# Optimization experiments

Hardware: AMD Instinct MI355X
Metric: run time of the kernel (lower is better)

The kernel has to match this reference:

```python
import jax, jax.numpy as jnp
import numpy as np

B, C_IN, L = 64, 8, 8192
ENC, K, CD = 64, 128, 64  # encoder_dim, codebook_size, code_dim


def setup_inputs() -> dict:
    key = jax.random.key(0)
    ks = jax.random.split(key, 12)
    u = lambda k, s, lim: jax.random.uniform(k, s, jnp.float32, -lim, lim)
    return {
        "x": jax.random.normal(ks[0], (B, C_IN, L), jnp.float32),
        "conv1_w": u(ks[1], (32, C_IN, 5), 1.0 / np.sqrt(C_IN * 5)),
        "conv1_b": u(ks[2], (32,), 1.0 / np.sqrt(C_IN * 5)),
        "conv2_w": u(ks[3], (ENC, 32, 5), 1.0 / np.sqrt(32 * 5)),
        "conv2_b": u(ks[4], (ENC,), 1.0 / np.sqrt(32 * 5)),
        "codebook": jax.random.uniform(ks[5], (K, CD), jnp.float32, -0.1, 0.1),
        "gru_w_ih": u(ks[6], (3 * ENC, CD), 1.0 / np.sqrt(ENC)),
        "gru_w_hh": u(ks[7], (3 * ENC, ENC), 1.0 / np.sqrt(ENC)),
        "gru_b_ih": u(ks[8], (3 * ENC,), 1.0 / np.sqrt(ENC)),
        "gru_b_hh": u(ks[9], (3 * ENC,), 1.0 / np.sqrt(ENC)),
        "proj_w": u(ks[10], (CD, ENC), 1.0 / np.sqrt(ENC)),
        "proj_b": u(ks[11], (CD,), 1.0 / np.sqrt(ENC)),
    }


def _conv1d(x, w, b):
    # x: [B, Cin, L], w: [Cout, Cin, 5], stride 2, padding 2
    y = jax.lax.conv_general_dilated(
        x, w, window_strides=(2,), padding=[(2, 2)],
        dimension_numbers=("NCH", "OIH", "NCH"))
    return y + b[None, :, None]


def _quantize(z, codebook):
    # z: [B, T, D]; squared-distance argmin + straight-through
    Bz, T, D = z.shape
    flat = z.reshape(Bz * T, D)
    flat_sg = jax.lax.stop_gradient(flat)
    cb_sg = jax.lax.stop_gradient(codebook)
    dist = ((flat_sg ** 2).sum(-1, keepdims=True)
            + (cb_sg ** 2).sum(-1)[None, :]
            - 2.0 * flat_sg @ cb_sg.T)  # [B*T, K]
    codes = jnp.argmin(dist, axis=1).reshape(Bz, T)
    quant = codebook[codes]  # [B, T, D]
    quant_z = z + jax.lax.stop_gradient(quant - z)
    return quant_z, codes


def _gru(seq, w_ih, w_hh, b_ih, b_hh):
    # seq: [B, T, CD] -> outputs [B, T, ENC]; torch GRU gate math
    Bz, T, _ = seq.shape
    H = w_hh.shape[1]
    x_proj = seq @ w_ih.T + b_ih  # [B, T, 3H]
    x_proj = jnp.transpose(x_proj, (1, 0, 2))  # [T, B, 3H]

    def step(h, xt):
        gh = h @ w_hh.T + b_hh
        xr, xz, xn = jnp.split(xt, 3, axis=-1)
        hr, hz, hn = jnp.split(gh, 3, axis=-1)
        r = jax.nn.sigmoid(xr + hr)
        zg = jax.nn.sigmoid(xz + hz)
        n = jnp.tanh(xn + r * hn)
        h_new = (1.0 - zg) * n + zg * h
        return h_new, h_new

    h0 = jnp.zeros((Bz, H), seq.dtype)
    _, hs = jax.lax.scan(step, h0, x_proj)
    return jnp.transpose(hs, (1, 0, 2))  # [B, T, H]


def reference(x, conv1_w, conv1_b, conv2_w, conv2_b, codebook,
              gru_w_ih, gru_w_hh, gru_b_ih, gru_b_hh, proj_w, proj_b):
    z = jax.nn.relu(_conv1d(x, conv1_w, conv1_b))
    z = jax.nn.relu(_conv1d(z, conv2_w, conv2_b))
    z = jnp.transpose(z, (0, 2, 1))  # [B, T, ENC]
    quant_z, codes = _quantize(z, codebook)
    ctx = _gru(quant_z, gru_w_ih, gru_w_hh, gru_b_ih, gru_b_hh)
    pred = ctx @ proj_w.T + proj_b
    return quant_z, pred, codes
```

## Files before the change

kernel.cpp:

```cpp
#include <hip/hip_runtime.h>

#define NB   64
#define CIN  8
#define LIN  8192
#define L1N  4096
#define T2   2048
#define ENC  64
#define NK   128
#define CD   64
#define G3   192

#define QOFF 0
#define POFF 8388608
#define COFF 16777216

#define PCOFF 128
#define CIOFF 24704

typedef _Float16 half2v __attribute__((ext_vector_type(2)));

__device__ __forceinline__ float sigf(float x) {
  float e = __builtin_amdgcn_exp2f(-1.4426950408889634f * x);
  return __builtin_amdgcn_rcpf(1.0f + e);
}
__device__ __forceinline__ float tanhf_fast(float x) {
  float e = __builtin_amdgcn_exp2f(2.8853900817779268f * x);
  return 1.0f - 2.0f * __builtin_amdgcn_rcpf(e + 1.0f);
}
__device__ __forceinline__ float rlane(float v, int k) {
  return __int_as_float(__builtin_amdgcn_readlane(__float_as_int(v), k));
}
__device__ __forceinline__ half2v as_h2(float v) { return __builtin_bit_cast(half2v, v); }

__global__ __launch_bounds__(192) void prep_kernel(const float* __restrict__ cb,
                                                   const float* __restrict__ w_ih,
                                                   const float* __restrict__ b_ih,
                                                   float* __restrict__ cnorm,
                                                   float* __restrict__ PC) {
  int blk = blockIdx.x;
  int j = threadIdx.x;
  if (blk == 128) {
    if (j < 128) {
      const float4* r = (const float4*)(cb + j * CD);
      float s0 = 0.f, s1 = 0.f, s2 = 0.f, s3 = 0.f;
#pragma unroll
      for (int q = 0; q < 16; q += 4) {
        float4 a = r[q], b = r[q + 1], cc = r[q + 2], d = r[q + 3];
        s0 += a.x * a.x + a.y * a.y + a.z * a.z + a.w * a.w;
        s1 += b.x * b.x + b.y * b.y + b.z * b.z + b.w * b.w;
        s2 += cc.x * cc.x + cc.y * cc.y + cc.z * cc.z + cc.w * cc.w;
        s3 += d.x * d.x + d.y * d.y + d.z * d.z + d.w * d.w;
      }
      cnorm[j] = (s0 + s1) + (s2 + s3);
    }
    return;
  }
  int c = blk;
  const float4* wp = (const float4*)(w_ih + j * ENC);
  const float4* cp = (const float4*)(cb + c * CD);
  float a0 = b_ih[j], a1 = 0.f, a2 = 0.f, a3 = 0.f;
#pragma unroll
  for (int q = 0; q < 16; q += 4) {
    float4 w0 = wp[q], c0 = cp[q];
    float4 w1 = wp[q + 1], c1 = cp[q + 1];
    float4 w2 = wp[q + 2], c2 = cp[q + 2];
    float4 w3 = wp[q + 3], c3 = cp[q + 3];
    a0 += w0.x * c0.x + w0.y * c0.y + w0.z * c0.z + w0.w * c0.w;
    a1 += w1.x * c1.x + w1.y * c1.y + w1.z * c1.z + w1.w * c1.w;
    a2 += w2.x * c2.x + w2.y * c2.y + w2.z * c2.z + w2.w * c2.w;
    a3 += w3.x * c3.x + w3.y * c3.y + w3.z * c3.z + w3.w * c3.w;
  }
  PC[c * G3 + j] = (a0 + a1) + (a2 + a3);
}

__global__ __launch_bounds__(256) void conv1_kernel(const float* __restrict__ x,
                                                    const float* __restrict__ w1,
                                                    const float* __restrict__ b1,
                                                    float* __restrict__ y1) {
  __shared__ float sw[1280];
  __shared__ float sx[8][136];
  int b = blockIdx.x >> 6;
  int t0 = (blockIdx.x & 63) * 64;
  int tid = threadIdx.x;
  for (int i = tid; i < 1280; i += 256) sw[i] = w1[i];
  const float* xb = x + b * CIN * LIN;
  for (int i = tid; i < 8 * 131; i += 256) {
    int ci = i / 131, u = i - ci * 131;
    int xi = 2 * t0 - 2 + u;
    sx[ci][u] = ((unsigned)xi < (unsigned)LIN) ? xb[ci * LIN + xi] : 0.f;
  }
  __syncthreads();
  int co = tid >> 3, tg = tid & 7;
  float bias = b1[co];
  float acc[8];
#pragma unroll
  for (int j = 0; j < 8; j++) acc[j] = bias;
#pragma unroll
  for (int ci = 0; ci < 8; ci++) {
    float xv[20];
    const float2* s2 = (const float2*)(&sx[ci][16 * tg]);
#pragma unroll
    for (int q = 0; q < 10; q++) {
      float2 v = s2[q];
      xv[2 * q] = v.x; xv[2 * q + 1] = v.y;
    }
    float wk[5];
#pragma unroll
    for (int k = 0; k < 5; k++) wk[k] = sw[(co * 8 + ci) * 5 + k];
#pragma unroll
    for (int j = 0; j < 8; j++) {
#pragma unroll
      for (int k = 0; k < 5; k++) acc[j] = fmaf(xv[2 * j + k], wk[k], acc[j]);
    }
  }
  float4* outp = (float4*)(y1 + (b * 32 + co) * L1N + t0 + tg * 8);
  float4 o0, o1;
  o0.x = fmaxf(acc[0], 0.f); o0.y = fmaxf(acc[1], 0.f);
  o0.z = fmaxf(acc[2], 0.f); o0.w = fmaxf(acc[3], 0.f);
  o1.x = fmaxf(acc[4], 0.f); o1.y = fmaxf(acc[5], 0.f);
  o1.z = fmaxf(acc[6], 0.f); o1.w = fmaxf(acc[7], 0.f);
  outp[0] = o0; outp[1] = o1;
}

__global__ __launch_bounds__(256) void conv2q_kernel(const float* __restrict__ y1,
                                                     const float* __restrict__ w2,
                                                     const float* __restrict__ b2,
                                                     const float* __restrict__ cb,
                                                     const float* __restrict__ cnorm,
                                                     float* __restrict__ quant,
                                                     float* __restrict__ codes_f,
                                                     int* __restrict__ codes_i) {
  __shared__ float sw[32 * 5 * 64];
  __shared__ float sx[32][136];
  __shared__ float sz[64][64];
  int b = blockIdx.x >> 5;
  int t0 = (blockIdx.x & 31) * 64;
  int tid = threadIdx.x;
  for (int i = tid; i < 32 * 5 * 64; i += 256) {
    int co = i & 63, r = i >> 6;
    sw[i] = w2[co * 160 + r];
  }
  for (int i = tid; i < 32 * 136; i += 256) {
    int ci = i / 136, u = i - ci * 136;
    int xi = 2 * t0 - 4 + u;
    float v = 0.f;
    if (xi >= 0 && xi < L1N) v = y1[(b * 32 + ci) * L1N + xi];
    sx[ci][u] = v;
  }
  __syncthreads();
  int co = tid & 63, ts = tid >> 6;
  float acc[16];
  float bb = b2[co];
#pragma unroll
  for (int i = 0; i < 16; i++) acc[i] = bb;
  for (int ci = 0; ci < 32; ci++) {
    float xr[40];
    const float4* sx4 = (const float4*)(&sx[ci][32 * ts]);
#pragma unroll
    for (int q = 0; q < 10; q++) {
      float4 v = sx4[q];
      xr[4 * q] = v.x; xr[4 * q + 1] = v.y; xr[4 * q + 2] = v.z; xr[4 * q + 3] = v.w;
    }
    float wk[5];
#pragma unroll
    for (int k = 0; k < 5; k++) wk[k] = sw[(ci * 5 + k) * 64 + co];
#pragma unroll
    for (int i = 0; i < 16; i++) {
#pragma unroll
      for (int k = 0; k < 5; k++) acc[i] = fmaf(xr[2 * i + k + 2], wk[k], acc[i]);
    }
  }
#pragma unroll
  for (int i = 0; i < 16; i++) sz[ts * 16 + i][co] = fmaxf(acc[i], 0.f);
  __syncthreads();

  int lane = co, wave = ts;
  float4 ca[16], cq[16];
  {
    const float4* pa = (const float4*)(cb + lane * CD);
    const float4* pb = (const float4*)(cb + (64 + lane) * CD);
#pragma unroll
    for (int q = 0; q < 16; q++) { ca[q] = pa[q]; cq[q] = pb[q]; }
  }
  float cn0 = cnorm[lane], cn1 = cnorm[64 + lane];
  int vg0 = b * T2 + t0 + wave * 16;
  for (int i = 0; i < 16; i++) {
    int vl = wave * 16 + i;
    int v = vg0 + i;
    float d00 = 0.f, d01 = 0.f, d02 = 0.f, d03 = 0.f;
    float d10 = 0.f, d11 = 0.f, d12 = 0.f, d13 = 0.f;
#pragma unroll
    for (int q = 0; q < 16; q++) {
      float4 zq = *(const float4*)(&sz[vl][4 * q]);
      d00 = fmaf(ca[q].x, zq.x, d00); d01 = fmaf(ca[q].y, zq.y, d01);
      d02 = fmaf(ca[q].z, zq.z, d02); d03 = fmaf(ca[q].w, zq.w, d03);
      d10 = fmaf(cq[q].x, zq.x, d10); d11 = fmaf(cq[q].y, zq.y, d11);
      d12 = fmaf(cq[q].z, zq.z, d12); d13 = fmaf(cq[q].w, zq.w, d13);
    }
    float s0 = cn0 - 2.f * ((d00 + d01) + (d02 + d03));
    float s1 = cn1 - 2.f * ((d10 + d11) + (d12 + d13));
    float sc; int idx;
    if (s1 < s0) { sc = s1; idx = 64 + lane; } else { sc = s0; idx = lane; }
#pragma unroll
    for (int m = 1; m < 64; m <<= 1) {
      float os = __shfl_xor(sc, m);
      int oi = __shfl_xor(idx, m);
      if (os < sc || (os == sc && oi < idx)) { sc = os; idx = oi; }
    }
    if (lane == 0) { codes_f[v] = (float)idx; codes_i[v] = idx; }
    quant[v * 64 + lane] = cb[idx * 64 + lane];
  }
}

__global__ __attribute__((amdgpu_flat_work_group_size(256, 256), amdgpu_waves_per_eu(1, 1)))
void gruproj_kernel(const float* __restrict__ PC,
                    const int* __restrict__ codes_i,
                    const float* __restrict__ w_hh,
                    const float* __restrict__ b_hh,
                    const float* __restrict__ proj_w,
                    const float* __restrict__ proj_b,
                    float* __restrict__ pred) {
  __shared__ float pcl[NK * G3];
  __shared__ int   cpl[T2];
  __shared__ float hring[2][16][64];
  int b = blockIdx.x;
  int tid = threadIdx.x;
  int lane = tid & 63;
  int wq = tid >> 6;

  {
    const int4* src = (const int4*)(codes_i + b * T2);
    int4* dst = (int4*)cpl;
    for (int f = tid; f < T2 / 4; f += 256) dst[f] = src[f];
    const float4* s2 = (const float4*)PC;
    float4* d2 = (float4*)pcl;
    for (int f = tid; f < NK * G3 / 4; f += 256) d2[f] = s2[f];
  }
  __syncthreads();

  half2v wr[32], wz[32], wn[32];
  float br = 0.f, bz = 0.f, bn = 0.f;
  float hreg = 0.f;
  int c2 = 0;
  float xr0 = 0.f, xz0 = 0.f, xn0 = 0.f, xr1 = 0.f, xz1 = 0.f, xn1 = 0.f;
  float4 w[16];
  float pbias = 0.f;

  if (wq == 0) {
    const float2* p0 = (const float2*)(w_hh + lane * ENC);
    const float2* p1 = (const float2*)(w_hh + (64 + lane) * ENC);
    const float2* p2 = (const float2*)(w_hh + (128 + lane) * ENC);
#pragma unroll
    for (int m = 0; m < 32; m++) {
      float2 a = p0[m]; wr[m] = (half2v){(_Float16)a.x, (_Float16)a.y};
      float2 c = p1[m]; wz[m] = (half2v){(_Float16)c.x, (_Float16)c.y};
      float2 d = p2[m]; wn[m] = (half2v){(_Float16)d.x, (_Float16)d.y};
    }
    br = b_hh[lane]; bz = b_hh[64 + lane]; bn = b_hh[128 + lane];
    c2 = cpl[2];
    int c0 = cpl[0], c1 = cpl[1];
    const float* g = pcl + c0 * G3;
    xr0 = g[lane]; xz0 = g[64 + lane]; xn0 = g[128 + lane];
    g = pcl + c1 * G3;
    xr1 = g[lane]; xz1 = g[64 + lane]; xn1 = g[128 + lane];
  } else {
    const float4* wp = (const float4*)(proj_w + lane * ENC);
#pragma unroll
    for (int q = 0; q < 16; q++) w[q] = wp[q];
    pbias = proj_b[lane];
  }

  int lane2a = 2 * lane, lane2b = 2 * lane + 1;
  const int cmax = T2 - 1;
  float* pbase = pred + (size_t)b * T2 * ENC + lane;

#pragma unroll 1
  for (int c = 0; c < 128; c++) {
    if (wq == 0) {
#pragma unroll 1
      for (int i = 0; i < 16; i++) {
        int t = c * 16 + i;
        const float* g = pcl + c2 * G3;
        float xr2 = g[lane], xz2 = g[64 + lane], xn2 = g[128 + lane];
        int tn = t + 3; if (tn > cmax) tn = cmax;
        c2 = cpl[tn];
        float he = __shfl(hreg, lane2a);
        float ho = __shfl(hreg, lane2b);
        half2v hp2 = {(_Float16)he, (_Float16)ho};
        float hpk = __builtin_bit_cast(float, hp2);
        float fr0 = br, fr1 = 0.f, fr2 = 0.f, fr3 = 0.f;
        float fz0 = bz, fz1 = 0.f, fz2 = 0.f, fz3 = 0.f;
        float fn0 = bn, fn1 = 0.f, fn2 = 0.f, fn3 = 0.f;
#define MV(q) { \
    float s0 = rlane(hpk, 4 * (q) + 0); float s1 = rlane(hpk, 4 * (q) + 1); \
    float s2 = rlane(hpk, 4 * (q) + 2); float s3 = rlane(hpk, 4 * (q) + 3); \
    fr0 = __builtin_amdgcn_fdot2(wr[4 * (q) + 0], as_h2(s0), fr0, false); \
    fr1 = __builtin_amdgcn_fdot2(wr[4 * (q) + 1], as_h2(s1), fr1, false); \
    fr2 = __builtin_amdgcn_fdot2(wr[4 * (q) + 2], as_h2(s2), fr2, false); \
    fr3 = __builtin_amdgcn_fdot2(wr[4 * (q) + 3], as_h2(s3), fr3, false); \
    fz0 = __builtin_amdgcn_fdot2(wz[4 * (q) + 0], as_h2(s0), fz0, false); \
    fz1 = __builtin_amdgcn_fdot2(wz[4 * (q) + 1], as_h2(s1), fz1, false); \
    fz2 = __builtin_amdgcn_fdot2(wz[4 * (q) + 2], as_h2(s2), fz2, false); \
    fz3 = __builtin_amdgcn_fdot2(wz[4 * (q) + 3], as_h2(s3), fz3, false); \
    fn0 = __builtin_amdgcn_fdot2(wn[4 * (q) + 0], as_h2(s0), fn0, false); \
    fn1 = __builtin_amdgcn_fdot2(wn[4 * (q) + 1], as_h2(s1), fn1, false); \
    fn2 = __builtin_amdgcn_fdot2(wn[4 * (q) + 2], as_h2(s2), fn2, false); \
    fn3 = __builtin_amdgcn_fdot2(wn[4 * (q) + 3], as_h2(s3), fn3, false); }
        MV(0) MV(1) MV(2) MV(3) MV(4) MV(5) MV(6) MV(7)
#undef MV
        float ghr = (fr0 + fr1) + (fr2 + fr3);
        float ghz = (fz0 + fz1) + (fz2 + fz3);
        float ghn = (fn0 + fn1) + (fn2 + fn3);
        float r = sigf(xr0 + ghr);
        float zg = sigf(xz0 + ghz);
        float n = tanhf_fast(xn0 + r * ghn);
        hreg = fmaf(zg, hreg - n, n);
        hring[c & 1][i][lane] = hreg;
        xr0 = xr1; xz0 = xz1; xn0 = xn1;
        xr1 = xr2; xz1 = xz2; xn1 = xn2;
      }
    } else if (c > 0) {
      int cc = c - 1, buf = cc & 1, tb = cc * 16;
#pragma unroll 1
      for (int t = wq - 1; t < 16; t += 3) {
        const float4* hrow = (const float4*)(&hring[buf][t][0]);
        float a0 = pbias, a1 = 0.f, a2 = 0.f, a3 = 0.f;
#pragma unroll
        for (int q = 0; q < 16; q += 4) {
          float4 ha = hrow[q], hb = hrow[q + 1], hc = hrow[q + 2], hd = hrow[q + 3];
          a0 += ha.x * w[q].x + ha.y * w[q].y + ha.z * w[q].z + ha.w * w[q].w;
          a1 += hb.x * w[q + 1].x + hb.y * w[q + 1].y + hb.z * w[q + 1].z + hb.w * w[q + 1].w;
          a2 += hc.x * w[q + 2].x + hc.y * w[q + 2].y + hc.z * w[q + 2].z + hc.w * w[q + 2].w;
          a3 += hd.x * w[q + 3].x + hd.y * w[q + 3].y + hd.z * w[q + 3].z + hd.w * w[q + 3].w;
        }
        pbase[(size_t)(tb + t) * ENC] = (a0 + a1) + (a2 + a3);
      }
    }
    __syncthreads();
  }
  if (wq > 0) {
    int cc = 127, buf = cc & 1, tb = cc * 16;
#pragma unroll 1
    for (int t = wq - 1; t < 16; t += 3) {
      const float4* hrow = (const float4*)(&hring[buf][t][0]);
      float a0 = pbias, a1 = 0.f, a2 = 0.f, a3 = 0.f;
#pragma unroll
      for (int q = 0; q < 16; q += 4) {
        float4 ha = hrow[q], hb = hrow[q + 1], hc = hrow[q + 2], hd = hrow[q + 3];
        a0 += ha.x * w[q].x + ha.y * w[q].y + ha.z * w[q].z + ha.w * w[q].w;
        a1 += hb.x * w[q + 1].x + hb.y * w[q + 1].y + hb.z * w[q + 1].z + hb.w * w[q + 1].w;
        a2 += hc.x * w[q + 2].x + hc.y * w[q + 2].y + hc.z * w[q + 2].z + hc.w * w[q + 2].w;
        a3 += hd.x * w[q + 3].x + hd.y * w[q + 3].y + hd.z * w[q + 3].z + hd.w * w[q + 3].w;
      }
      pbase[(size_t)(tb + t) * ENC] = (a0 + a1) + (a2 + a3);
    }
  }
}

extern "C" void kernel_launch(void* const* d_in, const int* in_sizes, int n_in,
                              void* d_out, int out_size, void* d_ws, size_t ws_size,
                              hipStream_t stream) {
  const float* x        = (const float*)d_in[0];
  const float* conv1_w  = (const float*)d_in[1];
  const float* conv1_b  = (const float*)d_in[2];
  const float* conv2_w  = (const float*)d_in[3];
  const float* conv2_b  = (const float*)d_in[4];
  const float* codebook = (const float*)d_in[5];
  const float* gru_w_ih = (const float*)d_in[6];
  const float* gru_w_hh = (const float*)d_in[7];
  const float* gru_b_ih = (const float*)d_in[8];
  const float* gru_b_hh = (const float*)d_in[9];
  const float* proj_w   = (const float*)d_in[10];
  const float* proj_b   = (const float*)d_in[11];

  float* out = (float*)d_out;
  float* quant = out + QOFF;
  float* predz = out + POFF;
  float* codes_f = out + COFF;

  float* ws = (float*)d_ws;
  float* cnorm = ws;
  float* PC = ws + PCOFF;
  int* codes_i = (int*)(ws + CIOFF);

  prep_kernel<<<129, 192, 0, stream>>>(codebook, gru_w_ih, gru_b_ih, cnorm, PC);
  conv1_kernel<<<4096, 256, 0, stream>>>(x, conv1_w, conv1_b, predz );
  conv2q_kernel<<<2048, 256, 0, stream>>>(predz , conv2_w, conv2_b, codebook, cnorm,
                                          quant, codes_f, codes_i);
  gruproj_kernel<<<64, 256, 0, stream>>>(PC, codes_i, gru_w_hh, gru_b_hh, proj_w, proj_b,
                                         predz );
}
```

Before: 1.119 ms.

## Fuse conv1 into conv2+quantize kernel to drop intermediate global round-trip

Merges the first convolution into the conv2/quantize kernel. Each block loads its raw input window with halo, computes the needed conv1 outputs (with recompute at tile edges) into shared memory, then runs conv2 and the codebook search as before. This removes the 64 MB intermediate write and read through global memory and one kernel launch. In exchange it adds some redundant halo compute, uses more shared memory per block, which may lower occupancy, and conv1 now runs on a smaller grid.

```diff
diff --git a/kernel.cpp b/kernel.cpp
--- a/kernel.cpp
+++ b/kernel.cpp
@@ -73,105 +73,101 @@
   PC[c * G3 + j] = (a0 + a1) + (a2 + a3);
 }
 
-__global__ __launch_bounds__(256) void conv1_kernel(const float* __restrict__ x,
-                                                    const float* __restrict__ w1,
-                                                    const float* __restrict__ b1,
-                                                    float* __restrict__ y1) {
-  __shared__ float sw[1280];
-  __shared__ float sx[8][136];
-  int b = blockIdx.x >> 6;
-  int t0 = (blockIdx.x & 63) * 64;
-  int tid = threadIdx.x;
-  for (int i = tid; i < 1280; i += 256) sw[i] = w1[i];
-  const float* xb = x + b * CIN * LIN;
-  for (int i = tid; i < 8 * 131; i += 256) {
-    int ci = i / 131, u = i - ci * 131;
-    int xi = 2 * t0 - 2 + u;
-    sx[ci][u] = ((unsigned)xi < (unsigned)LIN) ? xb[ci * LIN + xi] : 0.f;
-  }
-  __syncthreads();
-  int co = tid >> 3, tg = tid & 7;
-  float bias = b1[co];
-  float acc[8];
-#pragma unroll
-  for (int j = 0; j < 8; j++) acc[j] = bias;
-#pragma unroll
-  for (int ci = 0; ci < 8; ci++) {
-    float xv[20];
-    const float2* s2 = (const float2*)(&sx[ci][16 * tg]);
-#pragma unroll
-    for (int q = 0; q < 10; q++) {
-      float2 v = s2[q];
-      xv[2 * q] = v.x; xv[2 * q + 1] = v.y;
-    }
-    float wk[5];
-#pragma unroll
-    for (int k = 0; k < 5; k++) wk[k] = sw[(co * 8 + ci) * 5 + k];
-#pragma unroll
-    for (int j = 0; j < 8; j++) {
-#pragma unroll
-      for (int k = 0; k < 5; k++) acc[j] = fmaf(xv[2 * j + k], wk[k], acc[j]);
-    }
-  }
-  float4* outp = (float4*)(y1 + (b * 32 + co) * L1N + t0 + tg * 8);
-  float4 o0, o1;
-  o0.x = fmaxf(acc[0], 0.f); o0.y = fmaxf(acc[1], 0.f);
-  o0.z = fmaxf(acc[2], 0.f); o0.w = fmaxf(acc[3], 0.f);
-  o1.x = fmaxf(acc[4], 0.f); o1.y = fmaxf(acc[5], 0.f);
-  o1.z = fmaxf(acc[6], 0.f); o1.w = fmaxf(acc[7], 0.f);
-  outp[0] = o0; outp[1] = o1;
-}
-
-__global__ __launch_bounds__(256) void conv2q_kernel(const float* __restrict__ y1,
-                                                     const float* __restrict__ w2,
-                                                     const float* __restrict__ b2,
-                                                     const float* __restrict__ cb,
-                                                     const float* __restrict__ cnorm,
-                                                     float* __restrict__ quant,
-                                                     float* __restrict__ codes_f,
-                                                     int* __restrict__ codes_i) {
-  __shared__ float sw[32 * 5 * 64];
-  __shared__ float sx[32][136];
-  __shared__ float sz[64][64];
+__global__ __launch_bounds__(256) void conv12q_kernel(const float* __restrict__ x,
+                                                      const float* __restrict__ w1,
+                                                      const float* __restrict__ b1,
+                                                      const float* __restrict__ w2,
+                                                      const float* __restrict__ b2,
+                                                      const float* __restrict__ cb,
+                                                      const float* __restrict__ cnorm,
+                                                      float* __restrict__ quant,
+                                                      float* __restrict__ codes_f,
+                                                      int* __restrict__ codes_i) {
+  __shared__ float sw2[32 * 5 * 64];
+  __shared__ float sw1[1280];
+  __shared__ float sy[32][136];
+  __shared__ float ubuf[4096];
+  float (*sxx)[280] = (float(*)[280])ubuf;
+  float (*sz)[64]   = (float(*)[64])ubuf;
   int b = blockIdx.x >> 5;
   int t0 = (blockIdx.x & 31) * 64;
   int tid = threadIdx.x;
+
   for (int i = tid; i < 32 * 5 * 64; i += 256) {
     int co = i & 63, r = i >> 6;
-    sw[i] = w2[co * 160 + r];
-  }
-  for (int i = tid; i < 32 * 136; i += 256) {
-    int ci = i / 136, u = i - ci * 136;
-    int xi = 2 * t0 - 4 + u;
-    float v = 0.f;
-    if (xi >= 0 && xi < L1N) v = y1[(b * 32 + ci) * L1N + xi];
-    sx[ci][u] = v;
+    sw2[i] = w2[co * 160 + r];
+  }
+  for (int i = tid; i < 1280; i += 256) sw1[i] = w1[i];
+  {
+    const float* xb = x + b * CIN * LIN;
+    int X0 = 4 * t0 - 10;
+    for (int i = tid; i < 8 * 280; i += 256) {
+      int ci = i / 280, xo = i - ci * 280;
+      int xi = X0 + xo;
+      sxx[ci][xo] = ((unsigned)xi < (unsigned)LIN) ? xb[ci * LIN + xi] : 0.f;
+    }
   }
   __syncthreads();
+
+  {
+    int co1 = tid >> 3, sub = tid & 7;
+    float acc1[17];
+    float bias = b1[co1];
+#pragma unroll
+    for (int jj = 0; jj < 17; jj++) acc1[jj] = bias;
+#pragma unroll 1
+    for (int ci = 0; ci < 8; ci++) {
+      float xv[38];
+      const float2* s2 = (const float2*)(&sxx[ci][34 * sub]);
+#pragma unroll
+      for (int q = 0; q < 19; q++) {
+        float2 v = s2[q];
+        xv[2 * q] = v.x; xv[2 * q + 1] = v.y;
+      }
+      float wk1[5];
+#pragma unroll
+      for (int k = 0; k < 5; k++) wk1[k] = sw1[(co1 * 8 + ci) * 5 + k];
+#pragma unroll
+      for (int jj = 0; jj < 17; jj++) {
+#pragma unroll
+        for (int k = 0; k < 5; k++) acc1[jj] = fmaf(xv[2 * jj + k], wk1[k], acc1[jj]);
+      }
+    }
+#pragma unroll
+    for (int jj = 0; jj < 17; jj++) {
+      int u = 17 * sub + jj;
+      int p = 2 * t0 - 4 + u;
+      sy[co1][u] = ((unsigned)p < (unsigned)L1N) ? fmaxf(acc1[jj], 0.f) : 0.f;
+    }
+  }
+  __syncthreads();
+
   int co = tid & 63, ts = tid >> 6;
-  float acc[16];
-  float bb = b2[co];
-#pragma unroll
-  for (int i = 0; i < 16; i++) acc[i] = bb;
-  for (int ci = 0; ci < 32; ci++) {
-    float xr[40];
-    const float4* sx4 = (const float4*)(&sx[ci][32 * ts]);
-#pragma unroll
-    for (int q = 0; q < 10; q++) {
-      float4 v = sx4[q];
-      xr[4 * q] = v.x; xr[4 * q + 1] = v.y; xr[4 * q + 2] = v.z; xr[4 * q + 3] = v.w;
-    }
-    float wk[5];
-#pragma unroll
-    for (int k = 0; k < 5; k++) wk[k] = sw[(ci * 5 + k) * 64 + co];
-#pragma unroll
-    for (int i = 0; i < 16; i++) {
-#pragma unroll
-      for (int k = 0; k < 5; k++) acc[i] = fmaf(xr[2 * i + k + 2], wk[k], acc[i]);
-    }
-  }
-#pragma unroll
-  for (int i = 0; i < 16; i++) sz[ts * 16 + i][co] = fmaxf(acc[i], 0.f);
+  {
+    float acc[16];
+    float bb = b2[co];
+#pragma unroll
+    for (int i = 0; i < 16; i++) acc[i] = bb;
+    for (int ci = 0; ci < 32; ci++) {
+      float xr[40];
+      const float4* sx4 = (const float4*)(&sy[ci][32 * ts]);
+#pragma unroll
+      for (int q = 0; q < 10; q++) {
+        float4 v = sx4[q];
+        xr[4 * q] = v.x; xr[4 * q + 1] = v.y; xr[4 * q + 2] = v.z; xr[4 * q + 3] = v.w;
+      }
+      float wk[5];
+#pragma unroll
+      for (int k = 0; k < 5; k++) wk[k] = sw2[(ci * 5 + k) * 64 + co];
+#pragma unroll
+      for (int i = 0; i < 16; i++) {
+#pragma unroll
+        for (int k = 0; k < 5; k++) acc[i] = fmaf(xr[2 * i + k + 2], wk[k], acc[i]);
+      }
+    }
+#pragma unroll
+    for (int i = 0; i < 16; i++) sz[ts * 16 + i][co] = fmaxf(acc[i], 0.f);
+  }
   __syncthreads();
 
   int lane = co, wave = ts;
@@ -375,7 +371,7 @@
 
   float* out = (float*)d_out;
   float* quant = out + QOFF;
-  float* predz = out + POFF;
+  float* pred  = out + POFF;
   float* codes_f = out + COFF;
 
   float* ws = (float*)d_ws;
@@ -384,9 +380,7 @@
   int* codes_i = (int*)(ws + CIOFF);
 
   prep_kernel<<<129, 192, 0, stream>>>(codebook, gru_w_ih, gru_b_ih, cnorm, PC);
-  conv1_kernel<<<4096, 256, 0, stream>>>(x, conv1_w, conv1_b, predz );
-  conv2q_kernel<<<2048, 256, 0, stream>>>(predz , conv2_w, conv2_b, codebook, cnorm,
-                                          quant, codes_f, codes_i);
-  gruproj_kernel<<<64, 256, 0, stream>>>(PC, codes_i, gru_w_hh, gru_b_hh, proj_w, proj_b,
-                                         predz );
-}
+  conv12q_kernel<<<2048, 256, 0, stream>>>(x, conv1_w, conv1_b, conv2_w, conv2_b,
+                                           codebook, cnorm, quant, codes_f, codes_i);
+  gruproj_kernel<<<64, 256, 0, stream>>>(PC, codes_i, gru_w_hh, gru_b_hh, proj_w, proj_b, pred);
+}
```

Measured after the change: 1.101 ms. Within noise of the previous version (-1.5%).
